# Optimization experiments

Hardware: AMD Instinct MI355X
Metric: run time of the kernel (lower is better)

## Reference

```python
import jax, jax.numpy as jnp
import numpy as np

N_CLASSES = 8  # hardcoded by the (-1, 8, 8) reshape in the original layer

def setup_inputs() -> dict:
    key = jax.random.key(0)
    k1, k2, k3, k4 = jax.random.split(key, 4)
    B, F, C, R = 16384, 128, N_CLASSES, 64
    x = jax.random.normal(k1, (B, F), dtype=jnp.float32)
    p = jax.random.uniform(k2, (B, C), dtype=jnp.float32)  # class-prob-like input
    W = jax.random.normal(k3, (F, C * C, R), dtype=jnp.float32) * 0.02
    b = jax.random.normal(k4, (C, C, R), dtype=jnp.float32) * 0.1
    return {"x": x, "p": p, "W": W, "b": b}

def reference(x, p, W, b):
    # x: (B, 128) features; p: (B, C) class probs; W: (128, C*C, R); b: (C, C, R)
    B = x.shape[0]
    C = b.shape[0]
    R = b.shape[-1]
    # per-annotator GEMM fused across all annotators: (B, C*C, R)
    logits = jnp.einsum('bf,fkr->bkr', x, W).reshape(B, C, C, R) + b[None]
    # row-softmax: softmax over the "predicted class" axis for each true class c
    M = jax.nn.softmax(logits, axis=2)  # (B, C, C, R)
    # batched dot: p (B,C) contracted against rows of each annotator matrix
    out = jnp.einsum('bc,bcdr->bdr', p, M)  # (B, C, R)
    # NOTE: original applies K.dropout(0.5) (training-mode); omitted for a
    # deterministic inference reference (identity at eval).
    return out
```

## Files before the change

### kernel.cpp

```cpp
#include <hip/hip_runtime.h>
#include <hip/hip_bf16.h>


#define B_ROWS   16384
#define F_DIM    128
#define NCOL     4096
#define OUT_STRIDE 512
#define LOG2E    1.44269504088896340736f

typedef __bf16 bf16x8 __attribute__((ext_vector_type(8)));
typedef float  f32x4  __attribute__((ext_vector_type(4)));

#define AS1(p) ((const __attribute__((address_space(1))) unsigned int*)(p))
#define AS3(p) ((__attribute__((address_space(3))) unsigned int*)(p))

template <int CTRL>
__device__ __forceinline__ float dpp_add(float s) {
    int si = __builtin_bit_cast(int, s);
    int pi = __builtin_amdgcn_update_dpp(0, si, CTRL, 0xf, 0xf, true);
    return s + __builtin_bit_cast(float, pi);
}

__device__ __forceinline__ float swz4(float v) {
    return __builtin_bit_cast(float,
        __builtin_amdgcn_ds_swizzle(__builtin_bit_cast(int, v), 0x101F));
}


__global__ void wconv_kernel(const float* __restrict__ W, __bf16* __restrict__ wf) {
    int f    = blockIdx.x * 256 + threadIdx.x;
    int lane = f & 63;
    int tkk  = f >> 6;
    int T    = tkk >> 2;
    int kk   = tkk & 3;
    int c    = T >> 5;
    int w    = (T >> 3) & 3;
    int i    = T & 7;
    int col4 = lane & 15;
    int d    = (col4 & 3) | ((col4 >> 1) & 4);
    int r    = w * 16 + i * 2 + ((col4 >> 2) & 1);
    int n    = (c * 8 + d) * 64 + r;
    int kbase = kk * 32 + (lane >> 4) * 8;
    bf16x8 frag;
    for (int j = 0; j < 8; ++j)
        frag[j] = (__bf16)W[(kbase + j) * NCOL + n];
    *(bf16x8*)(wf + f * 8) = frag;
}

__global__ void bconv_kernel(const float* __restrict__ bias, float* __restrict__ bs) {
    int t    = blockIdx.x * 256 + threadIdx.x;
    int lane = t & 63;
    int T    = t >> 6;
    int c    = T >> 5;
    int w    = (T >> 3) & 3;
    int i    = T & 7;
    int col4 = lane & 15;
    int d    = (col4 & 3) | ((col4 >> 1) & 4);
    int r    = w * 16 + i * 2 + ((col4 >> 2) & 1);
    bs[t] = bias[(c * 8 + d) * 64 + r] * LOG2E;
}

__global__ __launch_bounds__(256, 4)
void fused_kernel(const float* __restrict__ x, const float* __restrict__ p,
                  const float* __restrict__ bs, const __bf16* __restrict__ wf,
                  float* __restrict__ out) {
    __shared__ __align__(16) char lds[32768 + 2048];

    const int lane = threadIdx.x & 63;
    const int ww   = threadIdx.x >> 6;
    const int quad = lane >> 4;
    const int l15  = lane & 15;
    const int w    = blockIdx.x & 3;
    const int b0   = (blockIdx.x >> 2) * 64 + ww * 16;
    const int d    = (l15 & 3) | ((l15 >> 1) & 4);
    const int rb   = (l15 >> 2) & 1;

    bf16x8 afr[4];
    {
        const float* xr = x + (b0 + l15) * F_DIM + quad * 8;
#pragma unroll
        for (int kk = 0; kk < 4; ++kk) {
            float4 lo = *(const float4*)(xr + kk * 32);
            float4 hi = *(const float4*)(xr + kk * 32 + 4);
            bf16x8 f;
            f[0] = (__bf16)lo.x; f[1] = (__bf16)lo.y;
            f[2] = (__bf16)lo.z; f[3] = (__bf16)lo.w;
            f[4] = (__bf16)hi.x; f[5] = (__bf16)hi.y;
            f[6] = (__bf16)hi.z; f[7] = (__bf16)hi.w;
            afr[kk] = f;
        }
    }

    float O_all[8][4] = {};

#pragma unroll 1
    for (int c = 0; c < 8; ++c) {
        {
            const __bf16* gbase = wf + (size_t)(c * 128 + w * 32) * 512 + lane * 8;
#pragma unroll
            for (int j = 0; j < 8; ++j) {
                int f = ww * 8 + j;
                __builtin_amdgcn_global_load_lds(AS1(gbase + f * 512),
                                                 AS3(lds + f * 1024), 16, 0, 0);
            }
            if (ww == 0) {
                const float* gb = bs + (c * 32 + w * 8) * 64 + lane * 4;
#pragma unroll
                for (int h = 0; h < 2; ++h)
                    __builtin_amdgcn_global_load_lds(AS1(gb + h * 256),
                                                     AS3(lds + 32768 + h * 1024), 16, 0, 0);
            }
        }
        __syncthreads();

        float pvv[4];
#pragma unroll
        for (int jj = 0; jj < 4; ++jj)
            pvv[jj] = p[(b0 + quad * 4 + jj) * 8 + c];

#pragma unroll
        for (int i = 0; i < 8; ++i) {
            f32x4 acc = {0.f, 0.f, 0.f, 0.f};
#pragma unroll
            for (int kk = 0; kk < 4; ++kk) {
                bf16x8 bfr = *(const bf16x8*)(lds + (i * 4 + kk) * 1024 + lane * 16);
                acc = __builtin_amdgcn_mfma_f32_16x16x32_bf16(afr[kk], bfr, acc, 0, 0, 0);
            }
            float bvl = *(const float*)(lds + 32768 + (i * 64 + lane) * 4);
#pragma unroll
            for (int jj = 0; jj < 4; ++jj) {
                float e = __builtin_amdgcn_exp2f(
                              __builtin_fmaf(acc[jj], LOG2E, bvl));
                float s = dpp_add<0xB1>(e);
                s = dpp_add<0x4E>(s);
                s = dpp_add<0x128>(s);
                O_all[i][jj] = __builtin_fmaf(
                    e, pvv[jj] * __builtin_amdgcn_rcpf(s), O_all[i][jj]);
            }
        }
        __syncthreads();
    }

    const bool bhi = (rb != 0);
#pragma unroll
    for (int jj = 0; jj < 4; ++jj) {
        float S[8];
#pragma unroll
        for (int i = 0; i < 8; ++i)
            S[i] = swz4(O_all[i][jj]);
        float T[8];
#pragma unroll
        for (int m = 0; m < 8; ++m) {
            int ilo = m >> 1, ihi = 4 + (m >> 1);
            float tlo = (m & 1) ? S[ilo]         : O_all[ilo][jj];
            float thi = (m & 1) ? O_all[ihi][jj] : S[ihi];
            T[m] = bhi ? thi : tlo;
        }
        float* orow = out + (b0 + quad * 4 + jj) * OUT_STRIDE
                          + d * 64 + w * 16 + rb * 8;
        f32x4 v0 = {T[0], T[1], T[2], T[3]};
        f32x4 v1 = {T[4], T[5], T[6], T[7]};
        *(f32x4*)(orow)     = v0;
        *(f32x4*)(orow + 4) = v1;
    }
}

extern "C" void kernel_launch(void* const* d_in, const int* in_sizes, int n_in,
                              void* d_out, int out_size, void* d_ws, size_t ws_size,
                              hipStream_t stream) {
    const float* x    = (const float*)d_in[0];
    const float* p    = (const float*)d_in[1];
    const float* W    = (const float*)d_in[2];
    const float* bias = (const float*)d_in[3];
    float* out = (float*)d_out;
    __bf16* wf = (__bf16*)d_ws;
    float*  bs = (float*)((char*)d_ws + (1 << 20));

    wconv_kernel<<<dim3(256), dim3(256), 0, stream>>>(W, wf);
    bconv_kernel<<<dim3(64), dim3(256), 0, stream>>>(bias, bs);
    fused_kernel<<<dim3(1024), dim3(256), 0, stream>>>(x, p, bs, wf, out);
}
```

Baseline: 111.4 us.

## Double-buffer weight tiles in LDS and process two row tiles per wave

The fused kernel now prefetches the next class's weight tile into a second LDS buffer while computing on the current one. It also drops the trailing barrier. Each wave handles two 16-row M tiles, so every B fragment read from LDS feeds two MFMAs, halving weight restaging per output row, and the grid shrinks to 512 blocks. Bias is read directly from global memory instead of being staged in LDS. The costs are more registers (launch bounds lowered to 2), half as many blocks, and possible lower occupancy, plus a question of whether the async LDS loads are properly waited on before use.

Measured after the change: 114.4 us. +2.7%, slower.

```diff
diff --git a/kernel.cpp b/kernel.cpp
--- a/kernel.cpp
+++ b/kernel.cpp
@@ -60,24 +60,25 @@
     bs[t] = bias[(c * 8 + d) * 64 + r] * LOG2E;
 }
 
-__global__ __launch_bounds__(256, 4)
+__global__ __launch_bounds__(256, 2)
 void fused_kernel(const float* __restrict__ x, const float* __restrict__ p,
                   const float* __restrict__ bs, const __bf16* __restrict__ wf,
                   float* __restrict__ out) {
-    __shared__ __align__(16) char lds[32768 + 2048];
+    __shared__ __align__(16) char lds[2][32768];
 
     const int lane = threadIdx.x & 63;
     const int ww   = threadIdx.x >> 6;
     const int quad = lane >> 4;
     const int l15  = lane & 15;
     const int w    = blockIdx.x & 3;
-    const int b0   = (blockIdx.x >> 2) * 64 + ww * 16;
+    const int b0   = (blockIdx.x >> 2) * 128 + ww * 32;
     const int d    = (l15 & 3) | ((l15 >> 1) & 4);
     const int rb   = (l15 >> 2) & 1;
 
-    bf16x8 afr[4];
-    {
-        const float* xr = x + (b0 + l15) * F_DIM + quad * 8;
+    bf16x8 afr[2][4];
+#pragma unroll
+    for (int mt = 0; mt < 2; ++mt) {
+        const float* xr = x + (b0 + mt * 16 + l15) * F_DIM + quad * 8;
 #pragma unroll
         for (int kk = 0; kk < 4; ++kk) {
             float4 lo = *(const float4*)(xr + kk * 32);
@@ -87,81 +88,92 @@
             f[2] = (__bf16)lo.z; f[3] = (__bf16)lo.w;
             f[4] = (__bf16)hi.x; f[5] = (__bf16)hi.y;
             f[6] = (__bf16)hi.z; f[7] = (__bf16)hi.w;
-            afr[kk] = f;
+            afr[mt][kk] = f;
         }
     }
 
-    float O_all[8][4] = {};
+    auto stage = [&](int c, char* dst) {
+        const __bf16* gbase = wf + (size_t)(c * 128 + w * 32) * 512 + lane * 8;
+#pragma unroll
+        for (int j = 0; j < 8; ++j) {
+            int f = ww * 8 + j;
+            __builtin_amdgcn_global_load_lds(AS1(gbase + f * 512),
+                                             AS3(dst + f * 1024), 16, 0, 0);
+        }
+    };
+
+    float O_all[2][8][4] = {};
+
+    stage(0, lds[0]);
 
 #pragma unroll 1
     for (int c = 0; c < 8; ++c) {
-        {
-            const __bf16* gbase = wf + (size_t)(c * 128 + w * 32) * 512 + lane * 8;
+        __syncthreads();
+        if (c < 7) stage(c + 1, lds[(c + 1) & 1]);
+        const char* buf = lds[c & 1];
+
+        float pvv[2][4];
 #pragma unroll
-            for (int j = 0; j < 8; ++j) {
-                int f = ww * 8 + j;
-                __builtin_amdgcn_global_load_lds(AS1(gbase + f * 512),
-                                                 AS3(lds + f * 1024), 16, 0, 0);
-            }
-            if (ww == 0) {
-                const float* gb = bs + (c * 32 + w * 8) * 64 + lane * 4;
+        for (int mt = 0; mt < 2; ++mt)
 #pragma unroll
-                for (int h = 0; h < 2; ++h)
-                    __builtin_amdgcn_global_load_lds(AS1(gb + h * 256),
-                                                     AS3(lds + 32768 + h * 1024), 16, 0, 0);
-            }
-        }
-        __syncthreads();
-
-        float pvv[4];
-#pragma unroll
-        for (int jj = 0; jj < 4; ++jj)
-            pvv[jj] = p[(b0 + quad * 4 + jj) * 8 + c];
+            for (int jj = 0; jj < 4; ++jj)
+                pvv[mt][jj] = p[(b0 + mt * 16 + quad * 4 + jj) * 8 + c];
 
 #pragma unroll
         for (int i = 0; i < 8; ++i) {
-            f32x4 acc = {0.f, 0.f, 0.f, 0.f};
+            bf16x8 bfr[4];
+#pragma unroll
+            for (int kk = 0; kk < 4; ++kk)
+                bfr[kk] = *(const bf16x8*)(buf + (i * 4 + kk) * 1024 + lane * 16);
+            f32x4 acc0 = {0.f, 0.f, 0.f, 0.f};
+            f32x4 acc1 = {0.f, 0.f, 0.f, 0.f};
 #pragma unroll
             for (int kk = 0; kk < 4; ++kk) {
-                bf16x8 bfr = *(const bf16x8*)(lds + (i * 4 + kk) * 1024 + lane * 16);
-                acc = __builtin_amdgcn_mfma_f32_16x16x32_bf16(afr[kk], bfr, acc, 0, 0, 0);
+                acc0 = __builtin_amdgcn_mfma_f32_16x16x32_bf16(afr[0][kk], bfr[kk], acc0, 0, 0, 0);
+                acc1 = __builtin_amdgcn_mfma_f32_16x16x32_bf16(afr[1][kk], bfr[kk], acc1, 0, 0, 0);
             }
-            float bvl = *(const float*)(lds + 32768 + (i * 64 + lane) * 4);
+            float bvl = bs[(c * 32 + w * 8 + i) * 64 + lane];
 #pragma unroll
-            for (int jj = 0; jj < 4; ++jj) {
-                float e = __builtin_amdgcn_exp2f(
-                              __builtin_fmaf(acc[jj], LOG2E, bvl));
-                float s = dpp_add<0xB1>(e);
-                s = dpp_add<0x4E>(s);
-                s = dpp_add<0x128>(s);
-                O_all[i][jj] = __builtin_fmaf(
-                    e, pvv[jj] * __builtin_amdgcn_rcpf(s), O_all[i][jj]);
+            for (int mt = 0; mt < 2; ++mt) {
+                const f32x4& acc = mt ? acc1 : acc0;
+#pragma unroll
+                for (int jj = 0; jj < 4; ++jj) {
+                    float e = __builtin_amdgcn_exp2f(
+                                  __builtin_fmaf(acc[jj], LOG2E, bvl));
+                    float s = dpp_add<0xB1>(e);
+                    s = dpp_add<0x4E>(s);
+                    s = dpp_add<0x128>(s);
+                    O_all[mt][i][jj] = __builtin_fmaf(
+                        e, pvv[mt][jj] * __builtin_amdgcn_rcpf(s), O_all[mt][i][jj]);
+                }
             }
         }
-        __syncthreads();
     }
 
     const bool bhi = (rb != 0);
 #pragma unroll
-    for (int jj = 0; jj < 4; ++jj) {
-        float S[8];
+    for (int mt = 0; mt < 2; ++mt) {
 #pragma unroll
-        for (int i = 0; i < 8; ++i)
-            S[i] = swz4(O_all[i][jj]);
-        float T[8];
+        for (int jj = 0; jj < 4; ++jj) {
+            float S[8];
 #pragma unroll
-        for (int m = 0; m < 8; ++m) {
-            int ilo = m >> 1, ihi = 4 + (m >> 1);
-            float tlo = (m & 1) ? S[ilo]         : O_all[ilo][jj];
-            float thi = (m & 1) ? O_all[ihi][jj] : S[ihi];
-            T[m] = bhi ? thi : tlo;
+            for (int i = 0; i < 8; ++i)
+                S[i] = swz4(O_all[mt][i][jj]);
+            float T[8];
+#pragma unroll
+            for (int m = 0; m < 8; ++m) {
+                int ilo = m >> 1, ihi = 4 + (m >> 1);
+                float tlo = (m & 1) ? S[ilo]             : O_all[mt][ilo][jj];
+                float thi = (m & 1) ? O_all[mt][ihi][jj] : S[ihi];
+                T[m] = bhi ? thi : tlo;
+            }
+            float* orow = out + (b0 + mt * 16 + quad * 4 + jj) * OUT_STRIDE
+                              + d * 64 + w * 16 + rb * 8;
+            f32x4 v0 = {T[0], T[1], T[2], T[3]};
+            f32x4 v1 = {T[4], T[5], T[6], T[7]};
+            *(f32x4*)(orow)     = v0;
+            *(f32x4*)(orow + 4) = v1;
         }
-        float* orow = out + (b0 + quad * 4 + jj) * OUT_STRIDE
-                          + d * 64 + w * 16 + rb * 8;
-        f32x4 v0 = {T[0], T[1], T[2], T[3]};
-        f32x4 v1 = {T[4], T[5], T[6], T[7]};
-        *(f32x4*)(orow)     = v0;
-        *(f32x4*)(orow + 4) = v1;
     }
 }
 
@@ -178,5 +190,5 @@
 
     wconv_kernel<<<dim3(256), dim3(256), 0, stream>>>(W, wf);
     bconv_kernel<<<dim3(64), dim3(256), 0, stream>>>(bias, bs);
-    fused_kernel<<<dim3(1024), dim3(256), 0, stream>>>(x, p, bs, wf, out);
+    fused_kernel<<<dim3(512), dim3(256), 0, stream>>>(x, p, bs, wf, out);
 }
```
